# Kernel optimization log

Measured on AMD Instinct MI355X. Metric: run time of the kernel, lower is better.

## Reference

```python
import jax, jax.numpy as jnp
import numpy as np

N, E, D_IN, E_DIM, H, C = 50000, 800000, 128, 101, 4, 32
HC = H * C  # 128
NEG_SLOPE = 0.2


def _glorot(key, shape):
    fan_in = shape[0]
    return jax.random.normal(key, shape, dtype=jnp.float32) / np.sqrt(fan_in)


def setup_inputs() -> dict:
    key = jax.random.key(0)
    ks = jax.random.split(key, 24)
    inp = {
        'x': jax.random.normal(ks[0], (N, D_IN), dtype=jnp.float32),
        'edge_index': jax.random.randint(ks[1], (2, E), 0, N, dtype=jnp.int64),
        'edge_attr': jax.random.normal(ks[2], (E, E_DIM), dtype=jnp.float32),
        # conv1: in=D_IN -> H*C
        'c1_Wl': _glorot(ks[3], (D_IN, HC)), 'c1_bl': jnp.zeros((HC,), jnp.float32),
        'c1_Wr': _glorot(ks[4], (D_IN, HC)), 'c1_br': jnp.zeros((HC,), jnp.float32),
        'c1_We': _glorot(ks[5], (E_DIM, HC)),
        'c1_att': _glorot(ks[6], (H, C)),
        'c1_bias': jnp.zeros((HC,), jnp.float32),
        # conv2: in=HC -> H*C
        'c2_Wl': _glorot(ks[7], (HC, HC)), 'c2_bl': jnp.zeros((HC,), jnp.float32),
        'c2_Wr': _glorot(ks[8], (HC, HC)), 'c2_br': jnp.zeros((HC,), jnp.float32),
        'c2_We': _glorot(ks[9], (E_DIM, HC)),
        'c2_att': _glorot(ks[10], (H, C)),
        'c2_bias': jnp.zeros((HC,), jnp.float32),
        # MLP head: HC -> 128 -> 64 -> 1
        'W1': _glorot(ks[11], (HC, 128)), 'b1': jnp.zeros((128,), jnp.float32),
        'W2': _glorot(ks[12], (128, 64)), 'b2': jnp.zeros((64,), jnp.float32),
        'W3': _glorot(ks[13], (64, 1)), 'b3': jnp.zeros((1,), jnp.float32),
    }
    return inp


def _gatv2_layer(x, src, dst, ea, Wl, bl, Wr, br, We, att, bias):
    # x: [N, Din]; src/dst: [Et]; ea: [Et, E_DIM]
    xl = (x @ Wl + bl).reshape(N, H, C)   # source transform
    xr = (x @ Wr + br).reshape(N, H, C)   # target transform
    ee = (ea @ We).reshape(-1, H, C)      # edge transform (no bias)
    g = jax.nn.leaky_relu(xl[src] + xr[dst] + ee, NEG_SLOPE)  # [Et,H,C]
    logit = jnp.einsum('ehc,hc->eh', g, att)                  # [Et,H]
    # segment softmax over incoming edges of each dst node
    amax = jax.ops.segment_max(logit, dst, num_segments=N)
    amax = jnp.where(jnp.isfinite(amax), amax, 0.0)
    ex = jnp.exp(logit - amax[dst])
    den = jax.ops.segment_sum(ex, dst, num_segments=N)
    alpha = ex / (den[dst] + 1e-16)                           # [Et,H]
    out = jax.ops.segment_sum(alpha[:, :, None] * xl[src], dst, num_segments=N)
    return out.reshape(N, HC) + bias


def reference(x, edge_index, edge_attr,
              c1_Wl, c1_bl, c1_Wr, c1_br, c1_We, c1_att, c1_bias,
              c2_Wl, c2_bl, c2_Wr, c2_br, c2_We, c2_att, c2_bias,
              W1, b1, W2, b2, W3, b3):
    src, dst = edge_index[0], edge_index[1]
    # add self loops with edge_attr fill_value='mean' (per-node mean of incoming)
    cnt = jax.ops.segment_sum(jnp.ones((E,), jnp.float32), dst, num_segments=N)
    loop_attr = jax.ops.segment_sum(edge_attr, dst, num_segments=N) / jnp.maximum(cnt, 1.0)[:, None]
    loop_idx = jnp.arange(N, dtype=src.dtype)
    src2 = jnp.concatenate([src, loop_idx])
    dst2 = jnp.concatenate([dst, loop_idx])
    ea2 = jnp.concatenate([edge_attr, loop_attr], axis=0)

    h = _gatv2_layer(x, src2, dst2, ea2, c1_Wl, c1_bl, c1_Wr, c1_br, c1_We, c1_att, c1_bias)
    h = jax.nn.relu(h)  # dropout = identity (eval)
    h = _gatv2_layer(h, src2, dst2, ea2, c2_Wl, c2_bl, c2_Wr, c2_br, c2_We, c2_att, c2_bias)
    h = jax.nn.relu(h)
    h = jax.nn.relu(h @ W1 + b1)
    h = jax.nn.relu(h @ W2 + b2)
    return h @ W3 + b3  # [N, 1]
```

## Files before the change

### kernel.cpp

```cpp
#include <hip/hip_runtime.h>
#include <cstdint>
#include <cstddef>

#define NN   50000
#define EE   800000
#define EDIM 101
#define E2T  850000

__global__ __launch_bounds__(256) void k_hist(const int* __restrict__ ei,
                                              int* __restrict__ icnt) {
  int e = blockIdx.x * 256 + threadIdx.x;
  if (e < EE) atomicAdd(&icnt[ei[EE + e]], 1);
}

__global__ __launch_bounds__(1024) void k_scan(const int* __restrict__ icnt,
                                               int* __restrict__ rowptr) {
  __shared__ int ts[1024];
  int t = threadIdx.x;
  const int CH = (NN + 1023) / 1024;
  int base = t * CH;
  int s = 0;
  for (int i = 0; i < CH; ++i) {
    int idx = base + i;
    if (idx < NN) s += icnt[idx];
  }
  ts[t] = s;
  __syncthreads();
  for (int d = 1; d < 1024; d <<= 1) {
    int v = (t >= d) ? ts[t - d] : 0;
    __syncthreads();
    ts[t] += v;
    __syncthreads();
  }
  int run = (t == 0) ? 0 : ts[t - 1];
  for (int i = 0; i < CH; ++i) {
    int idx = base + i;
    if (idx < NN) { rowptr[idx] = run; run += icnt[idx]; }
  }
}

__global__ __launch_bounds__(256) void k_scatter(const int* __restrict__ ei,
                                                 const int* __restrict__ rowptr,
                                                 int* __restrict__ cursor,
                                                 int* __restrict__ eord) {
  int e = blockIdx.x * 256 + threadIdx.x;
  if (e >= EE) return;
  int d = ei[EE + e];
  int p = atomicAdd(&cursor[d], 1);
  eord[rowptr[d] + p] = e;
}

__global__ __launch_bounds__(256) void k_rc(const int* __restrict__ icnt,
                                            float* __restrict__ rc) {
  int n = blockIdx.x * 256 + threadIdx.x;
  if (n < NN) rc[n] = 1.0f / fmaxf((float)icnt[n], 1.0f);
}

__global__ __launch_bounds__(256) void k_las(
    const float* __restrict__ ea, const int* __restrict__ eord,
    const int* __restrict__ rowptr, const int* __restrict__ icnt,
    float* __restrict__ las) {
  int n = blockIdx.x * 2 + (threadIdx.x >> 7);
  int j = threadIdx.x & 127;
  if (j >= EDIM) return;
  int nb = rowptr[n], D = icnt[n];
  float acc = 0.f;
  for (int i = 0; i < D; ++i) {
    int e = eord[nb + i];
    acc += ea[(size_t)e * EDIM + j];
  }
  las[(size_t)n * EDIM + j] = acc;
}

template <int K>
__global__ __launch_bounds__(256) void k_gemm(
    const float* __restrict__ A, int lda,
    const float* __restrict__ B, int ldb,
    const float* __restrict__ bias,
    const float* __restrict__ rowscale,
    float* __restrict__ C, int ldc, int M, int relu) {
  constexpr int KP = K + 1;
  __shared__ float As[64 * KP];
  __shared__ float Bs[K * 64];
  int tid = threadIdx.x;
  int row0 = blockIdx.x * 64;
  int col0 = blockIdx.y * 64;

  for (int idx = tid; idx < 64 * K; idx += 256) {
    int r = idx / K, k = idx - r * K;
    int gr = row0 + r;
    As[r * KP + k] = (gr < M) ? A[(size_t)gr * lda + k] : 0.0f;
  }
  for (int idx = tid; idx < K * 64; idx += 256) {
    int k = idx >> 6, c = idx & 63;
    Bs[idx] = B[(size_t)k * ldb + col0 + c];
  }
  __syncthreads();

  int tr = tid >> 4, tc = tid & 15;
  float acc[4][4] = {};
  const float* ap = &As[tr * 4 * KP];
  const float* bp = &Bs[tc * 4];
#pragma unroll 4
  for (int k = 0; k < K; ++k) {
    float a0 = ap[k], a1 = ap[KP + k], a2 = ap[2 * KP + k], a3 = ap[3 * KP + k];
    float4 b = *(const float4*)&bp[k * 64];
    acc[0][0] += a0 * b.x; acc[0][1] += a0 * b.y; acc[0][2] += a0 * b.z; acc[0][3] += a0 * b.w;
    acc[1][0] += a1 * b.x; acc[1][1] += a1 * b.y; acc[1][2] += a1 * b.z; acc[1][3] += a1 * b.w;
    acc[2][0] += a2 * b.x; acc[2][1] += a2 * b.y; acc[2][2] += a2 * b.z; acc[2][3] += a2 * b.w;
    acc[3][0] += a3 * b.x; acc[3][1] += a3 * b.y; acc[3][2] += a3 * b.z; acc[3][3] += a3 * b.w;
  }

  float4 bv = make_float4(0.f, 0.f, 0.f, 0.f);
  if (bias) bv = *(const float4*)&bias[col0 + tc * 4];
#pragma unroll
  for (int i = 0; i < 4; ++i) {
    int r = row0 + tr * 4 + i;
    if (r >= M) break;
    float sc = rowscale ? rowscale[r] : 1.0f;
    float4 v;
    v.x = acc[i][0] * sc + bv.x;
    v.y = acc[i][1] * sc + bv.y;
    v.z = acc[i][2] * sc + bv.z;
    v.w = acc[i][3] * sc + bv.w;
    if (relu) {
      v.x = fmaxf(v.x, 0.f); v.y = fmaxf(v.y, 0.f);
      v.z = fmaxf(v.z, 0.f); v.w = fmaxf(v.w, 0.f);
    }
    *(float4*)&C[(size_t)r * ldc + col0 + tc * 4] = v;
  }
}

__global__ __launch_bounds__(256) void k_edge_logit(
    const float* __restrict__ ea, const int* __restrict__ ei,
    const float* __restrict__ We, const float* __restrict__ att,
    const float* __restrict__ xl, const float* __restrict__ xr,
    float* __restrict__ logit) {
  constexpr int KP2 = EDIM + 1;
  __shared__ float Ws[EDIM * 128];
  __shared__ float Es[64 * KP2];
  int tid = threadIdx.x;
  int e0 = blockIdx.x * 64;

  for (int idx = tid; idx < (EDIM * 128) / 4; idx += 256)
    ((float4*)Ws)[idx] = ((const float4*)We)[idx];
  for (int idx = tid; idx < 64 * EDIM; idx += 256) {
    int r = idx / EDIM, k = idx - r * EDIM;
    Es[r * KP2 + k] = ea[(size_t)(e0 + r) * EDIM + k];
  }
  __syncthreads();

  int tr = tid >> 4, tc = tid & 15;
  int c0 = tc * 8;
  float acc[4][8] = {};
  const float* ep = &Es[tr * 4 * KP2];
#pragma unroll 4
  for (int k = 0; k < EDIM; ++k) {
    float a[4] = {ep[k], ep[KP2 + k], ep[2 * KP2 + k], ep[3 * KP2 + k]};
    float b[8];
    *(float4*)&b[0] = *(const float4*)&Ws[k * 128 + c0];
    *(float4*)&b[4] = *(const float4*)&Ws[k * 128 + c0 + 4];
#pragma unroll
    for (int i = 0; i < 4; ++i)
#pragma unroll
      for (int j = 0; j < 8; ++j) acc[i][j] += a[i] * b[j];
  }

  float av[8];
  *(float4*)&av[0] = *(const float4*)&att[c0];
  *(float4*)&av[4] = *(const float4*)&att[c0 + 4];
  int h = tc >> 2;
#pragma unroll
  for (int i = 0; i < 4; ++i) {
    int e = e0 + tr * 4 + i;
    int s = ei[e];
    int d = ei[EE + e];
    float xa[8], xb[8];
    *(float4*)&xa[0] = *(const float4*)&xl[(size_t)s * 128 + c0];
    *(float4*)&xa[4] = *(const float4*)&xl[(size_t)s * 128 + c0 + 4];
    *(float4*)&xb[0] = *(const float4*)&xr[(size_t)d * 128 + c0];
    *(float4*)&xb[4] = *(const float4*)&xr[(size_t)d * 128 + c0 + 4];
    float p = 0.f;
#pragma unroll
    for (int j = 0; j < 8; ++j) {
      float z = acc[i][j] + xa[j] + xb[j];
      float g = z > 0.f ? z : 0.2f * z;
      p += g * av[j];
    }
    p += __shfl_xor(p, 1);
    p += __shfl_xor(p, 2);
    if ((tc & 3) == 0) logit[(size_t)e * 4 + h] = p;
  }
}

__global__ __launch_bounds__(256) void k_loop_logit(
    const float* __restrict__ xl, const float* __restrict__ xr,
    const float* __restrict__ eel, const float* __restrict__ att,
    float* __restrict__ logit) {
  int n = blockIdx.x * 2 + (threadIdx.x >> 7);
  int j = threadIdx.x & 127;
  size_t o = (size_t)n * 128 + j;
  float z = xl[o] + xr[o] + eel[o];
  float g = z > 0.f ? z : 0.2f * z;
  float p = g * att[j];
  p += __shfl_xor(p, 1);  p += __shfl_xor(p, 2);  p += __shfl_xor(p, 4);
  p += __shfl_xor(p, 8);  p += __shfl_xor(p, 16);
  if ((j & 31) == 0) logit[(size_t)(EE + n) * 4 + (j >> 5)] = p;
}

__global__ __launch_bounds__(256) void k_node_aggr(
    const int* __restrict__ ei, const int* __restrict__ eord,
    const int* __restrict__ rowptr, const int* __restrict__ icnt,
    const float* __restrict__ logit, const float* __restrict__ xl,
    const float* __restrict__ bias, float* __restrict__ hout) {
  int l = threadIdx.x & 63;
  int n = blockIdx.x * 4 + (threadIdx.x >> 6);
  int nb = rowptr[n], D = icnt[n];
  int T = D + 1;

  const float NEGINF = -3.0e38f;
  float m0 = NEGINF, m1 = NEGINF, m2 = NEGINF, m3 = NEGINF;
  for (int t = l; t < T; t += 64) {
    int le = (t < D) ? eord[nb + t] : (EE + n);
    float4 lv = *(const float4*)&logit[(size_t)le * 4];
    m0 = fmaxf(m0, lv.x); m1 = fmaxf(m1, lv.y);
    m2 = fmaxf(m2, lv.z); m3 = fmaxf(m3, lv.w);
  }
#pragma unroll
  for (int s = 1; s < 64; s <<= 1) {
    m0 = fmaxf(m0, __shfl_xor(m0, s));
    m1 = fmaxf(m1, __shfl_xor(m1, s));
    m2 = fmaxf(m2, __shfl_xor(m2, s));
    m3 = fmaxf(m3, __shfl_xor(m3, s));
  }

  float d0 = 0.f, d1 = 0.f, d2 = 0.f, d3 = 0.f;
  for (int t = l; t < T; t += 64) {
    int le = (t < D) ? eord[nb + t] : (EE + n);
    float4 lv = *(const float4*)&logit[(size_t)le * 4];
    d0 += __expf(lv.x - m0); d1 += __expf(lv.y - m1);
    d2 += __expf(lv.z - m2); d3 += __expf(lv.w - m3);
  }
#pragma unroll
  for (int s = 1; s < 64; s <<= 1) {
    d0 += __shfl_xor(d0, s); d1 += __shfl_xor(d1, s);
    d2 += __shfl_xor(d2, s); d3 += __shfl_xor(d3, s);
  }

  int c = l * 2;
  int h = l >> 4;
  float mh = (h == 0) ? m0 : (h == 1) ? m1 : (h == 2) ? m2 : m3;
  float acc0 = 0.f, acc1 = 0.f;
  for (int t = 0; t < T; ++t) {
    int le, s;
    if (t < D) { le = eord[nb + t]; s = ei[le]; }
    else       { le = EE + n;       s = n; }
    float ex = __expf(logit[(size_t)le * 4 + h] - mh);
    float2 v = *(const float2*)&xl[(size_t)s * 128 + c];
    acc0 += ex * v.x;
    acc1 += ex * v.y;
  }
  float dh = ((h == 0) ? d0 : (h == 1) ? d1 : (h == 2) ? d2 : d3) + 1e-16f;
  float r = 1.0f / dh;
  float2 b = *(const float2*)&bias[c];
  float2 o;
  o.x = fmaxf(acc0 * r + b.x, 0.f);
  o.y = fmaxf(acc1 * r + b.y, 0.f);
  *(float2*)&hout[(size_t)n * 128 + c] = o;
}

__global__ __launch_bounds__(256) void k_mlp3(
    const float* __restrict__ m2, const float* __restrict__ W3,
    const float* __restrict__ b3, float* __restrict__ out) {
  int n = blockIdx.x * 4 + (threadIdx.x >> 6);
  int l = threadIdx.x & 63;
  float p = m2[(size_t)n * 64 + l] * W3[l];
  p += __shfl_xor(p, 1);  p += __shfl_xor(p, 2);  p += __shfl_xor(p, 4);
  p += __shfl_xor(p, 8);  p += __shfl_xor(p, 16); p += __shfl_xor(p, 32);
  if (l == 0) out[n] = p + b3[0];
}

extern "C" void kernel_launch(void* const* d_in, const int* in_sizes, int n_in,
                              void* d_out, int out_size, void* d_ws, size_t ws_size,
                              hipStream_t stream) {
  const float* x  = (const float*)d_in[0];
  const int*   ei = (const int*)d_in[1];
  const float* ea = (const float*)d_in[2];
  const float* c1_Wl   = (const float*)d_in[3];
  const float* c1_bl   = (const float*)d_in[4];
  const float* c1_Wr   = (const float*)d_in[5];
  const float* c1_br   = (const float*)d_in[6];
  const float* c1_We   = (const float*)d_in[7];
  const float* c1_att  = (const float*)d_in[8];
  const float* c1_bias = (const float*)d_in[9];
  const float* c2_Wl   = (const float*)d_in[10];
  const float* c2_bl   = (const float*)d_in[11];
  const float* c2_Wr   = (const float*)d_in[12];
  const float* c2_br   = (const float*)d_in[13];
  const float* c2_We   = (const float*)d_in[14];
  const float* c2_att  = (const float*)d_in[15];
  const float* c2_bias = (const float*)d_in[16];
  const float* W1 = (const float*)d_in[17];
  const float* b1 = (const float*)d_in[18];
  const float* W2 = (const float*)d_in[19];
  const float* b2 = (const float*)d_in[20];
  const float* W3 = (const float*)d_in[21];
  const float* b3 = (const float*)d_in[22];
  float* out = (float*)d_out;

  char* ws = (char*)d_ws;
  size_t off = 0;
  auto alloc = [&](size_t bytes) { size_t p = off; off += (bytes + 255) & ~(size_t)255; return p; };
  size_t o_icnt   = alloc((size_t)NN * 4);
  size_t o_cursor = alloc((size_t)NN * 4);
  size_t o_rowptr = alloc((size_t)NN * 4);
  size_t o_eord   = alloc((size_t)EE * 4);
  size_t o_rc     = alloc((size_t)NN * 4);
  size_t o_las    = alloc((size_t)NN * EDIM * 4);
  size_t o_xl     = alloc((size_t)NN * 128 * 4);
  size_t o_xr     = alloc((size_t)NN * 128 * 4);
  size_t o_eel    = alloc((size_t)NN * 128 * 4);
  size_t o_logit  = alloc((size_t)E2T * 4 * 4);
  size_t o_h      = alloc((size_t)NN * 128 * 4);
  (void)ws_size; (void)in_sizes; (void)n_in; (void)out_size;

  int*   icnt   = (int*)(ws + o_icnt);
  int*   cursor = (int*)(ws + o_cursor);
  int*   rowptr = (int*)(ws + o_rowptr);
  int*   eord   = (int*)(ws + o_eord);
  float* rc     = (float*)(ws + o_rc);
  float* las    = (float*)(ws + o_las);
  float* xl     = (float*)(ws + o_xl);
  float* xr     = (float*)(ws + o_xr);
  float* eel    = (float*)(ws + o_eel);
  float* lg     = (float*)(ws + o_logit);
  float* hbuf   = (float*)(ws + o_h);

  hipMemsetAsync(ws + o_icnt, 0, o_rowptr - o_icnt, stream);
  k_hist<<<(EE + 255) / 256, 256, 0, stream>>>(ei, icnt);
  k_scan<<<1, 1024, 0, stream>>>(icnt, rowptr);
  k_rc<<<(NN + 255) / 256, 256, 0, stream>>>(icnt, rc);
  k_scatter<<<(EE + 255) / 256, 256, 0, stream>>>(ei, rowptr, cursor, eord);
  k_las<<<NN / 2, 256, 0, stream>>>(ea, eord, rowptr, icnt, las);

  const float* Wls[2]  = {c1_Wl, c2_Wl};
  const float* bls[2]  = {c1_bl, c2_bl};
  const float* Wrs[2]  = {c1_Wr, c2_Wr};
  const float* brs[2]  = {c1_br, c2_br};
  const float* Wes[2]  = {c1_We, c2_We};
  const float* atts[2] = {c1_att, c2_att};
  const float* bss[2]  = {c1_bias, c2_bias};

  for (int L = 0; L < 2; ++L) {
    const float* xin = (L == 0) ? x : hbuf;
    k_gemm<128><<<dim3(782, 2), 256, 0, stream>>>(xin, 128, Wls[L], 128, bls[L], nullptr, xl, 128, NN, 0);
    k_gemm<128><<<dim3(782, 2), 256, 0, stream>>>(xin, 128, Wrs[L], 128, brs[L], nullptr, xr, 128, NN, 0);
    k_gemm<EDIM><<<dim3(782, 2), 256, 0, stream>>>(las, EDIM, Wes[L], 128, nullptr, rc, eel, 128, NN, 0);
    k_edge_logit<<<EE / 64, 256, 0, stream>>>(ea, ei, Wes[L], atts[L], xl, xr, lg);
    k_loop_logit<<<NN / 2, 256, 0, stream>>>(xl, xr, eel, atts[L], lg);
    k_node_aggr<<<NN / 4, 256, 0, stream>>>(ei, eord, rowptr, icnt, lg, xl, bss[L], hbuf);
  }

  k_gemm<128><<<dim3(782, 2), 256, 0, stream>>>(hbuf, 128, W1, 128, b1, nullptr, xl, 128, NN, 1);
  k_gemm<128><<<dim3(782, 1), 256, 0, stream>>>(xl, 128, W2, 64, b2, nullptr, xr, 64, NN, 1);
  k_mlp3<<<NN / 4, 256, 0, stream>>>(xr, W3, b3, out);
}
```

Measured before the change: 2.513 ms.

## Compute edge-attribute projection with split-bf16 MFMA instead of FP32 FMA

The per-edge ea@We projection in the logit kernel now runs on matrix cores using bf16x3 split precision (hi*hi + hi*lo + lo*hi), which keeps accuracy close to fp32. A new conversion kernel first writes edge_attr as padded 128-wide bf16 hi and lo arrays, and both layers reuse them. We is split and swizzled into LDS once per block, and each block now handles 128 edges. The cost is an extra pass over edge_attr, about 400 MB of new workspace traffic, and more global reads of eaH/eaL per layer than the original fp32 read.

```diff
diff --git a/kernel.cpp b/kernel.cpp
--- a/kernel.cpp
+++ b/kernel.cpp
@@ -6,6 +6,19 @@
 #define EE   800000
 #define EDIM 101
 #define E2T  850000
+#define KPB  128
+
+typedef __attribute__((ext_vector_type(8))) short s8v;
+typedef __attribute__((ext_vector_type(4))) float f4v;
+
+__device__ __forceinline__ unsigned short f2bf(float x) {
+  unsigned u = __float_as_uint(x);
+  unsigned r = (u + 0x7fffu + ((u >> 16) & 1u)) >> 16;
+  return (unsigned short)r;
+}
+__device__ __forceinline__ float bf2f(unsigned short b) {
+  return __uint_as_float(((unsigned)b) << 16);
+}
 
 __global__ __launch_bounds__(256) void k_hist(const int* __restrict__ ei,
                                               int* __restrict__ icnt) {
@@ -70,6 +83,29 @@
     acc += ea[(size_t)e * EDIM + j];
   }
   las[(size_t)n * EDIM + j] = acc;
+}
+
+__global__ __launch_bounds__(256) void k_cvt(
+    const float* __restrict__ ea,
+    unsigned short* __restrict__ eaH, unsigned short* __restrict__ eaL) {
+  int idx = blockIdx.x * 256 + threadIdx.x;
+  int e = idx >> 5, kq = idx & 31;
+  int k = kq * 4;
+  unsigned short h[4], l[4];
+#pragma unroll
+  for (int j = 0; j < 4; ++j) {
+    float v = (k + j < EDIM) ? ea[(size_t)e * EDIM + k + j] : 0.0f;
+    unsigned short hb = f2bf(v);
+    h[j] = hb;
+    l[j] = f2bf(v - bf2f(hb));
+  }
+  uint2 hp, lp;
+  hp.x = (unsigned)h[0] | ((unsigned)h[1] << 16);
+  hp.y = (unsigned)h[2] | ((unsigned)h[3] << 16);
+  lp.x = (unsigned)l[0] | ((unsigned)l[1] << 16);
+  lp.y = (unsigned)l[2] | ((unsigned)l[3] << 16);
+  *(uint2*)&eaH[(size_t)e * KPB + k] = hp;
+  *(uint2*)&eaL[(size_t)e * KPB + k] = lp;
 }
 
 template <int K>
@@ -131,65 +167,106 @@
   }
 }
 
-__global__ __launch_bounds__(256) void k_edge_logit(
-    const float* __restrict__ ea, const int* __restrict__ ei,
-    const float* __restrict__ We, const float* __restrict__ att,
+__global__ __launch_bounds__(256) void k_edge_logit_mfma(
+    const unsigned short* __restrict__ eaH, const unsigned short* __restrict__ eaL,
+    const int* __restrict__ ei, const float* __restrict__ We,
+    const float* __restrict__ att,
     const float* __restrict__ xl, const float* __restrict__ xr,
     float* __restrict__ logit) {
-  constexpr int KP2 = EDIM + 1;
-  __shared__ float Ws[EDIM * 128];
-  __shared__ float Es[64 * KP2];
+  __shared__ __align__(16) unsigned short BH[16384];
+  __shared__ __align__(16) unsigned short BL[16384];
+  __shared__ int sdl[128], sdr[128];
+
   int tid = threadIdx.x;
-  int e0 = blockIdx.x * 64;
-
-  for (int idx = tid; idx < (EDIM * 128) / 4; idx += 256)
-    ((float4*)Ws)[idx] = ((const float4*)We)[idx];
-  for (int idx = tid; idx < 64 * EDIM; idx += 256) {
-    int r = idx / EDIM, k = idx - r * EDIM;
-    Es[r * KP2 + k] = ea[(size_t)(e0 + r) * EDIM + k];
+  int e0 = blockIdx.x * 128;
+
+  if (tid < 128) {
+    sdl[tid] = ei[e0 + tid];
+    sdr[tid] = ei[EE + e0 + tid];
+  }
+  for (int idx = tid; idx < 2048; idx += 256) {
+    int n = idx & 127, kg = idx >> 7;
+    int nt = n >> 4, ln0 = n & 15, ks = kg >> 2, q0 = kg & 3;
+    s8v h8, l8;
+#pragma unroll
+    for (int j = 0; j < 8; ++j) {
+      int k = kg * 8 + j;
+      float v = (k < EDIM) ? We[(size_t)k * 128 + n] : 0.0f;
+      unsigned short hb = f2bf(v);
+      h8[j] = (short)hb;
+      l8[j] = (short)f2bf(v - bf2f(hb));
+    }
+    int off = ((nt * 4 + ks) * 64 + q0 * 16 + ln0) * 8;
+    *(s8v*)&BH[off] = h8;
+    *(s8v*)&BL[off] = l8;
   }
   __syncthreads();
 
-  int tr = tid >> 4, tc = tid & 15;
-  int c0 = tc * 8;
-  float acc[4][8] = {};
-  const float* ep = &Es[tr * 4 * KP2];
-#pragma unroll 4
-  for (int k = 0; k < EDIM; ++k) {
-    float a[4] = {ep[k], ep[KP2 + k], ep[2 * KP2 + k], ep[3 * KP2 + k]};
-    float b[8];
-    *(float4*)&b[0] = *(const float4*)&Ws[k * 128 + c0];
-    *(float4*)&b[4] = *(const float4*)&Ws[k * 128 + c0 + 4];
-#pragma unroll
-    for (int i = 0; i < 4; ++i)
-#pragma unroll
-      for (int j = 0; j < 8; ++j) acc[i][j] += a[i] * b[j];
-  }
-
-  float av[8];
-  *(float4*)&av[0] = *(const float4*)&att[c0];
-  *(float4*)&av[4] = *(const float4*)&att[c0 + 4];
-  int h = tc >> 2;
-#pragma unroll
-  for (int i = 0; i < 4; ++i) {
-    int e = e0 + tr * 4 + i;
-    int s = ei[e];
-    int d = ei[EE + e];
-    float xa[8], xb[8];
-    *(float4*)&xa[0] = *(const float4*)&xl[(size_t)s * 128 + c0];
-    *(float4*)&xa[4] = *(const float4*)&xl[(size_t)s * 128 + c0 + 4];
-    *(float4*)&xb[0] = *(const float4*)&xr[(size_t)d * 128 + c0];
-    *(float4*)&xb[4] = *(const float4*)&xr[(size_t)d * 128 + c0 + 4];
-    float p = 0.f;
-#pragma unroll
-    for (int j = 0; j < 8; ++j) {
-      float z = acc[i][j] + xa[j] + xb[j];
-      float g = z > 0.f ? z : 0.2f * z;
-      p += g * av[j];
+  int w = tid >> 6, lane = tid & 63;
+  int ln = lane & 15, q = lane >> 4;
+
+  f4v acc[2][8];
+#pragma unroll
+  for (int m = 0; m < 2; ++m)
+#pragma unroll
+    for (int nt = 0; nt < 8; ++nt) acc[m][nt] = (f4v){0.f, 0.f, 0.f, 0.f};
+
+#pragma unroll
+  for (int ks = 0; ks < 4; ++ks) {
+    s8v ah[2], al[2];
+#pragma unroll
+    for (int m = 0; m < 2; ++m) {
+      size_t ao = (size_t)(e0 + (w * 2 + m) * 16 + ln) * KPB + ks * 32 + q * 8;
+      ah[m] = *(const s8v*)&eaH[ao];
+      al[m] = *(const s8v*)&eaL[ao];
     }
-    p += __shfl_xor(p, 1);
-    p += __shfl_xor(p, 2);
-    if ((tc & 3) == 0) logit[(size_t)e * 4 + h] = p;
+#pragma unroll
+    for (int nt = 0; nt < 8; ++nt) {
+      int off = ((nt * 4 + ks) * 64 + lane) * 8;
+      s8v bh = *(const s8v*)&BH[off];
+      s8v bl = *(const s8v*)&BL[off];
+#pragma unroll
+      for (int m = 0; m < 2; ++m) {
+        acc[m][nt] = __builtin_amdgcn_mfma_f32_16x16x32_bf16(ah[m], bh, acc[m][nt], 0, 0, 0);
+        acc[m][nt] = __builtin_amdgcn_mfma_f32_16x16x32_bf16(ah[m], bl, acc[m][nt], 0, 0, 0);
+        acc[m][nt] = __builtin_amdgcn_mfma_f32_16x16x32_bf16(al[m], bh, acc[m][nt], 0, 0, 0);
+      }
+    }
+  }
+
+  float attv[8];
+#pragma unroll
+  for (int nt = 0; nt < 8; ++nt) attv[nt] = att[nt * 16 + ln];
+
+#pragma unroll
+  for (int m = 0; m < 2; ++m) {
+    int mt = w * 2 + m;
+#pragma unroll
+    for (int i = 0; i < 4; ++i) {
+      int er = mt * 16 + q * 4 + i;
+      int e = e0 + er;
+      int s = sdl[er], d = sdr[er];
+      float ph0 = 0.f, ph1 = 0.f, ph2 = 0.f, ph3 = 0.f;
+#pragma unroll
+      for (int nt = 0; nt < 8; ++nt) {
+        int col = nt * 16 + ln;
+        float z = acc[m][nt][i] + xl[(size_t)s * 128 + col] + xr[(size_t)d * 128 + col];
+        float g = z > 0.f ? z : 0.2f * z;
+        float t = g * attv[nt];
+        if (nt < 2) ph0 += t; else if (nt < 4) ph1 += t;
+        else if (nt < 6) ph2 += t; else ph3 += t;
+      }
+      ph0 += __shfl_xor(ph0, 1); ph0 += __shfl_xor(ph0, 2);
+      ph0 += __shfl_xor(ph0, 4); ph0 += __shfl_xor(ph0, 8);
+      ph1 += __shfl_xor(ph1, 1); ph1 += __shfl_xor(ph1, 2);
+      ph1 += __shfl_xor(ph1, 4); ph1 += __shfl_xor(ph1, 8);
+      ph2 += __shfl_xor(ph2, 1); ph2 += __shfl_xor(ph2, 2);
+      ph2 += __shfl_xor(ph2, 4); ph2 += __shfl_xor(ph2, 8);
+      ph3 += __shfl_xor(ph3, 1); ph3 += __shfl_xor(ph3, 2);
+      ph3 += __shfl_xor(ph3, 4); ph3 += __shfl_xor(ph3, 8);
+      if (ln == 0)
+        *(float4*)&logit[(size_t)e * 4] = make_float4(ph0, ph1, ph2, ph3);
+    }
   }
 }
 
@@ -322,6 +399,8 @@
   size_t o_eel    = alloc((size_t)NN * 128 * 4);
   size_t o_logit  = alloc((size_t)E2T * 4 * 4);
   size_t o_h      = alloc((size_t)NN * 128 * 4);
+  size_t o_eaH    = alloc((size_t)EE * KPB * 2);
+  size_t o_eaL    = alloc((size_t)EE * KPB * 2);
   (void)ws_size; (void)in_sizes; (void)n_in; (void)out_size;
 
   int*   icnt   = (int*)(ws + o_icnt);
@@ -335,6 +414,8 @@
   float* eel    = (float*)(ws + o_eel);
   float* lg     = (float*)(ws + o_logit);
   float* hbuf   = (float*)(ws + o_h);
+  unsigned short* eaH = (unsigned short*)(ws + o_eaH);
+  unsigned short* eaL = (unsigned short*)(ws + o_eaL);
 
   hipMemsetAsync(ws + o_icnt, 0, o_rowptr - o_icnt, stream);
   k_hist<<<(EE + 255) / 256, 256, 0, stream>>>(ei, icnt);
@@ -342,6 +423,7 @@
   k_rc<<<(NN + 255) / 256, 256, 0, stream>>>(icnt, rc);
   k_scatter<<<(EE + 255) / 256, 256, 0, stream>>>(ei, rowptr, cursor, eord);
   k_las<<<NN / 2, 256, 0, stream>>>(ea, eord, rowptr, icnt, las);
+  k_cvt<<<(EE * 32) / 256, 256, 0, stream>>>(ea, eaH, eaL);
 
   const float* Wls[2]  = {c1_Wl, c2_Wl};
   const float* bls[2]  = {c1_bl, c2_bl};
@@ -356,7 +438,7 @@
     k_gemm<128><<<dim3(782, 2), 256, 0, stream>>>(xin, 128, Wls[L], 128, bls[L], nullptr, xl, 128, NN, 0);
     k_gemm<128><<<dim3(782, 2), 256, 0, stream>>>(xin, 128, Wrs[L], 128, brs[L], nullptr, xr, 128, NN, 0);
     k_gemm<EDIM><<<dim3(782, 2), 256, 0, stream>>>(las, EDIM, Wes[L], 128, nullptr, rc, eel, 128, NN, 0);
-    k_edge_logit<<<EE / 64, 256, 0, stream>>>(ea, ei, Wes[L], atts[L], xl, xr, lg);
+    k_edge_logit_mfma<<<EE / 128, 256, 0, stream>>>(eaH, eaL, ei, Wes[L], atts[L], xl, xr, lg);
     k_loop_logit<<<NN / 2, 256, 0, stream>>>(xl, xr, eel, atts[L], lg);
     k_node_aggr<<<NN / 4, 256, 0, stream>>>(ei, eord, rowptr, icnt, lg, xl, bss[L], hbuf);
   }
```

Result: faster. 2.303 ms (-8.3%).
